# Kernel optimization log

Measured on AMD Instinct MI355X. Metric: run time of the kernel, lower is better.

Reference implementation:

```python
import jax, jax.numpy as jnp
import numpy as np

N, E, B, H = 20000, 100000, 512, 64
IN_CH, EDGE_DIM, OUT_CH = 16, 8, 1


def setup_inputs() -> dict:
    key = jax.random.key(0)
    ks = jax.random.split(key, 20)
    rn = lambda k, shp, s=0.1: (jax.random.normal(k, shp, jnp.float32) * s)
    return {
        'x': rn(ks[0], (N, IN_CH), 1.0),
        'edge_index': jax.random.randint(ks[1], (2, E), 0, N),
        'edge_attr': rn(ks[2], (E, EDGE_DIM), 1.0),
        'batch': jnp.sort(jax.random.randint(ks[3], (N,), 0, B)),
        'lin0_w': rn(ks[4], (IN_CH, H)), 'lin0_b': jnp.zeros((H,), jnp.float32),
        'nn1_w': rn(ks[5], (EDGE_DIM, 128)), 'nn1_b': jnp.zeros((128,), jnp.float32),
        'nn2_w': rn(ks[6], (128, H * H), 0.02), 'nn2_b': jnp.zeros((H * H,), jnp.float32),
        'root_w': rn(ks[7], (H, H)), 'root_b': jnp.zeros((H,), jnp.float32),
        'gru_wih': rn(ks[8], (H, 3 * H)), 'gru_whh': rn(ks[9], (H, 3 * H)),
        'gru_bih': jnp.zeros((3 * H,), jnp.float32), 'gru_bhh': jnp.zeros((3 * H,), jnp.float32),
        'lstm_wih': rn(ks[10], (2 * H, 4 * H)), 'lstm_whh': rn(ks[11], (H, 4 * H)),
        'lstm_bih': jnp.zeros((4 * H,), jnp.float32), 'lstm_bhh': jnp.zeros((4 * H,), jnp.float32),
        'lin1_w': rn(ks[12], (2 * H, H)), 'lin1_b': jnp.zeros((H,), jnp.float32),
        'lin2_w': rn(ks[13], (H, OUT_CH)), 'lin2_b': jnp.zeros((OUT_CH,), jnp.float32),
    }


def reference(x, edge_index, edge_attr, batch, lin0_w, lin0_b, nn1_w, nn1_b,
              nn2_w, nn2_b, root_w, root_b, gru_wih, gru_whh, gru_bih, gru_bhh,
              lstm_wih, lstm_whh, lstm_bih, lstm_bhh, lin1_w, lin1_b, lin2_w, lin2_b):
    src, dst = edge_index[0], edge_index[1]
    # edge network weights (shared across the 3 message-passing steps)
    ew = jax.nn.relu(edge_attr @ nn1_w + nn1_b) @ nn2_w + nn2_b  # [E, H*H]
    ew = ew.reshape(E, H, H)
    deg = jnp.maximum(jax.ops.segment_sum(jnp.ones((E,), x.dtype), dst, N), 1.0)

    out = jax.nn.relu(x @ lin0_w + lin0_b)  # [N, H]
    h = out
    for _ in range(3):
        # NNConv: gather src feats, per-edge matvec, scatter-mean to dst, + root linear
        msg = jnp.einsum('ei,eio->eo', out[src], ew)                  # [E, H]
        agg = jax.ops.segment_sum(msg, dst, N) / deg[:, None]          # [N, H]
        m = jax.nn.relu(agg + out @ root_w + root_b)
        # GRU cell (torch gate order r, z, n)
        gi = m @ gru_wih + gru_bih
        gh = h @ gru_whh + gru_bhh
        r = jax.nn.sigmoid(gi[:, :H] + gh[:, :H])
        z = jax.nn.sigmoid(gi[:, H:2 * H] + gh[:, H:2 * H])
        n = jnp.tanh(gi[:, 2 * H:] + r * gh[:, 2 * H:])
        h = (1.0 - z) * n + z * h
        out = h

    # Set2Set pooling, 3 processing steps (torch LSTM gate order i, f, g, o)
    q_star = jnp.zeros((B, 2 * H), x.dtype)
    hh = jnp.zeros((B, H), x.dtype)
    cc = jnp.zeros((B, H), x.dtype)
    for _ in range(3):
        g = q_star @ lstm_wih + hh @ lstm_whh + lstm_bih + lstm_bhh    # [B, 4H]
        i_g = jax.nn.sigmoid(g[:, :H])
        f_g = jax.nn.sigmoid(g[:, H:2 * H])
        g_g = jnp.tanh(g[:, 2 * H:3 * H])
        o_g = jax.nn.sigmoid(g[:, 3 * H:])
        cc = f_g * cc + i_g * g_g
        hh = o_g * jnp.tanh(cc)
        q = hh                                                          # [B, H]
        e = jnp.sum(out * q[batch], axis=-1)                            # [N]
        e_max = jax.ops.segment_max(e, batch, B)
        a = jnp.exp(e - e_max[batch])
        a = a / jax.ops.segment_sum(a, batch, B)[batch]
        rvec = jax.ops.segment_sum(a[:, None] * out, batch, B)          # [B, H]
        q_star = jnp.concatenate([q, rvec], axis=-1)

    y = jax.nn.relu(q_star @ lin1_w + lin1_b) @ lin2_w + lin2_b         # [B, 1]
    return y
```

## Files before the change

### kernel.cpp

```cpp
#include <hip/hip_runtime.h>
#include <hip/hip_bf16.h>
#include <hip/hip_fp16.h>
#include <cstddef>
#include <cstdint>

#define N_NODES 20000
#define N_EDGES 100000
#define N_BATCH 512

#define EPB 96
#define TS 6
#define ECAP 100032

typedef __attribute__((ext_vector_type(8))) short ushort8_t;
typedef __attribute__((ext_vector_type(8))) _Float16 f16x8;
typedef __attribute__((ext_vector_type(4))) float f32x4;

union F16x8U { f16x8 v; unsigned int u[4]; };

__device__ __forceinline__ float sigmoidf_(float x) { return 1.f / (1.f + expf(-x)); }
__device__ __forceinline__ unsigned short f2h(float x) {
    return __half_as_ushort(__float2half(x));
}
__device__ __forceinline__ float h2f(unsigned short s) {
    return __half2float(__ushort_as_half(s));
}

#define LIN0_BLOCKS 5000
#define BSW_BLOCKS 258
#define CNT_BLOCKS 391

__global__ __launch_bounds__(256) void prep1_kernel(
        const float* __restrict__ x, const float* __restrict__ l0w, const float* __restrict__ l0b,
        const float* __restrict__ w2, const float* __restrict__ b2,
        const int* __restrict__ ei,
        float* __restrict__ out, unsigned short* __restrict__ bsw,
        int* __restrict__ cnt, int E) {
    int bid = blockIdx.x, tid = threadIdx.x;
    if (bid < LIN0_BLOCKS) {
        int idx = bid * 256 + tid;
        int n = idx >> 6, j = idx & 63;
        float acc = l0b[j];
#pragma unroll
        for (int i = 0; i < 16; i++) acc += x[n * 16 + i] * l0w[i * 64 + j];
        out[idx] = fmaxf(acc, 0.f);
    } else if (bid < LIN0_BLOCKS + BSW_BLOCKS) {
        int idx = (bid - LIN0_BLOCKS) * 256 + tid;
        if (idx < 66048) {
            int l = idx & 63, oc = (idx >> 6) & 3, ks = idx >> 8;
            int o = oc * 16 + (l & 15);
            int kap0 = ks * 32 + 8 * (l >> 4);
#pragma unroll
            for (int j = 0; j < 8; ++j) {
                int kap = kap0 + j;
                int k = kap >> 6, i = kap & 63;
                float v = (k < 128) ? w2[(size_t)k * 4096 + i * 64 + o] : b2[i * 64 + o];
                bsw[(size_t)idx * 8 + j] = f2h(v);
            }
        }
    } else {
        int e = (bid - LIN0_BLOCKS - BSW_BLOCKS) * 256 + tid;
        if (e < E) atomicAdd(&cnt[ei[E + e]], 1);
    }
}

__global__ __launch_bounds__(1024) void scan_kernel(const int* __restrict__ cnt,
                                                    int* __restrict__ cstart,
                                                    int* __restrict__ cursor,
                                                    float* __restrict__ degf, int n) {
    __shared__ int part[1024];
    int t = threadIdx.x;
    int base = t * 20;
    int loc[20];
    int s = 0;
#pragma unroll
    for (int i = 0; i < 20; ++i) {
        int idx = base + i;
        int c = (idx < n) ? cnt[idx] : 0;
        loc[i] = s;
        s += c;
    }
    part[t] = s;
    __syncthreads();
    for (int off = 1; off < 1024; off <<= 1) {
        int v = (t >= off) ? part[t - off] : 0;
        __syncthreads();
        part[t] += v;
        __syncthreads();
    }
    int tb = part[t] - s;
#pragma unroll
    for (int i = 0; i < 20; ++i) {
        int idx = base + i;
        if (idx < n) {
            int b0 = tb + loc[i];
            cstart[idx] = b0;
            cursor[idx] = b0;
            degf[idx] = (float)cnt[idx];
        }
    }
}

__global__ void place_kernel(const int* __restrict__ ei, int* __restrict__ cursor,
                             int* __restrict__ eperm, int* __restrict__ src_s, int E) {
    int e = blockIdx.x * 256 + threadIdx.x;
    if (e < E) {
        int dst = ei[E + e];
        int slot = atomicAdd(&cursor[dst], 1);
        eperm[slot] = e;
        src_s[slot] = ei[e];
    }
}

__global__ __launch_bounds__(256) void hidden_kernel(const float* __restrict__ ea,
                                                     const float* __restrict__ w1,
                                                     const float* __restrict__ b1,
                                                     const int* __restrict__ eperm,
                                                     unsigned short* __restrict__ hb) {
    int idx = blockIdx.x * 256 + threadIdx.x;
    int s = idx >> 7, j = idx & 127;
    int e = eperm[s];
    float acc = b1[j];
#pragma unroll
    for (int i = 0; i < 8; i++) acc += ea[e * 8 + i] * w1[i * 128 + j];
    hb[idx] = f2h(fmaxf(acc, 0.f));
}

__global__ __launch_bounds__(256, 2) void msg_mfma(const float* __restrict__ out,
                                                   const unsigned short* __restrict__ hb,
                                                   const unsigned short* __restrict__ bsw,
                                                   const int* __restrict__ src_s,
                                                   unsigned short* __restrict__ msgp, int E) {
    __shared__ __align__(16) unsigned short hs16[128 * EPB];
    const int tid = threadIdx.x;
    const int w = tid >> 6, l = tid & 63;
    const int e0 = blockIdx.x * EPB;
    const int r16 = l & 15, q = l >> 4;

    if (tid < EPB) {
        int e = e0 + tid;
        bool v = e < E;
        const ushort8_t* hrow = (const ushort8_t*)(hb + (size_t)e * 128);
#pragma unroll
        for (int c = 0; c < 16; ++c) {
            ushort8_t hv = {};
            if (v) hv = hrow[c];
#pragma unroll
            for (int j = 0; j < 8; ++j)
                hs16[(c * 8 + j) * EPB + tid] = (unsigned short)hv[j];
        }
    }

    f16x8 sfrag[TS][2];
#pragma unroll
    for (int t = 0; t < TS; ++t) {
        int e = e0 + t * 16 + r16;
        int src = (e < E) ? src_s[e] : 0;
        const f32x4* p = (const f32x4*)(out + (size_t)src * 64);
#pragma unroll
        for (int st = 0; st < 2; ++st) {
            f16x8 f = {};
            if (e < E) {
                f32x4 a = p[st * 8 + q * 2], b = p[st * 8 + q * 2 + 1];
#pragma unroll
                for (int j = 0; j < 4; ++j) { f[j] = (_Float16)a[j]; f[4 + j] = (_Float16)b[j]; }
            }
            sfrag[t][st] = f;
        }
    }

    const f16x8* bp = (const f16x8*)bsw;
    f16x8 bfA[8], bfB[8];
#pragma unroll
    for (int i = 0; i < 8; ++i) bfA[i] = bp[((w * 8 + i) << 6) + l];

    __syncthreads();

    f32x4 acc[TS][4] = {};

#define MSG_COMPUTE(K, BF)                                                     \
    {                                                                          \
        _Pragma("unroll")                                                      \
        for (int t = 0; t < TS; ++t) {                                         \
            unsigned int hu = hs16[(K) * EPB + t * 16 + r16];                  \
            _Pragma("unroll")                                                  \
            for (int st = 0; st < 2; ++st) {                                   \
                F16x8U s_, a_;                                                 \
                s_.v = sfrag[t][st];                                           \
                asm("v_pk_mul_f16 %0, %1, %2 op_sel:[0,0] op_sel_hi:[0,1]"     \
                    : "=v"(a_.u[0]) : "v"(hu), "v"(s_.u[0]));                  \
                asm("v_pk_mul_f16 %0, %1, %2 op_sel:[0,0] op_sel_hi:[0,1]"     \
                    : "=v"(a_.u[1]) : "v"(hu), "v"(s_.u[1]));                  \
                asm("v_pk_mul_f16 %0, %1, %2 op_sel:[0,0] op_sel_hi:[0,1]"     \
                    : "=v"(a_.u[2]) : "v"(hu), "v"(s_.u[2]));                  \
                asm("v_pk_mul_f16 %0, %1, %2 op_sel:[0,0] op_sel_hi:[0,1]"     \
                    : "=v"(a_.u[3]) : "v"(hu), "v"(s_.u[3]));                  \
                _Pragma("unroll")                                              \
                for (int oc = 0; oc < 4; ++oc)                                 \
                    acc[t][oc] = __builtin_amdgcn_mfma_f32_16x16x32_f16(       \
                        a_.v, BF[st * 4 + oc], acc[t][oc], 0, 0, 0);           \
            }                                                                  \
        }                                                                      \
    }

#pragma unroll 1
    for (int kk = 0; kk < 16; ++kk) {
        int k1 = w + kk * 8;
        int k2 = k1 + 4;
#pragma unroll
        for (int i = 0; i < 8; ++i) bfB[i] = bp[((k2 * 8 + i) << 6) + l];
        MSG_COMPUTE(k1, bfA);
        if (kk < 15) {
            int k3 = k1 + 8;
#pragma unroll
            for (int i = 0; i < 8; ++i) bfA[i] = bp[((k3 * 8 + i) << 6) + l];
        }
        MSG_COMPUTE(k2, bfB);
    }
#undef MSG_COMPUTE

    if (w == 0) {
#pragma unroll
        for (int i = 0; i < 8; ++i) bfA[i] = bp[((128 * 8 + i) << 6) + l];
#pragma unroll
        for (int t = 0; t < TS; ++t)
#pragma unroll
            for (int st = 0; st < 2; ++st)
#pragma unroll
                for (int oc = 0; oc < 4; ++oc)
                    acc[t][oc] = __builtin_amdgcn_mfma_f32_16x16x32_f16(
                        sfrag[t][st], bfA[st * 4 + oc], acc[t][oc], 0, 0, 0);
    }

    unsigned short* slab = msgp + (size_t)w * ECAP * 64;
#pragma unroll
    for (int t = 0; t < TS; ++t) {
#pragma unroll
        for (int r = 0; r < 4; ++r) {
            int e = e0 + t * 16 + q * 4 + r;
            if (e < E) {
                unsigned short* row = slab + (size_t)e * 64 + r16;
                row[0]  = f2h(acc[t][0][r]);
                row[16] = f2h(acc[t][1][r]);
                row[32] = f2h(acc[t][2][r]);
                row[48] = f2h(acc[t][3][r]);
            }
        }
    }
}

__global__ __launch_bounds__(256) void gru_kernel(float* __restrict__ out,
                                                  const unsigned short* __restrict__ msgp,
                                                  const int* __restrict__ cstart,
                                                  const int* __restrict__ cnt,
                                                  const float* __restrict__ deg,
                                                  const float* __restrict__ root_w,
                                                  const float* __restrict__ root_b,
                                                  const float* __restrict__ wih,
                                                  const float* __restrict__ whh,
                                                  const float* __restrict__ bih,
                                                  const float* __restrict__ bhh) {
    int w = threadIdx.x >> 6, j = threadIdx.x & 63;
    int n = blockIdx.x * 4 + w;
    __shared__ float s_o[4][64];
    __shared__ float s_m[4][64];
    s_o[w][j] = out[(size_t)n * 64 + j];
    __syncthreads();

    float msum = 0.f;
    {
        int base = cstart[n], c = cnt[n];
        for (int s2 = 0; s2 < c; ++s2) {
            size_t slot = (size_t)(base + s2) * 64 + j;
            float a0 = h2f(msgp[slot]);
            float a1 = h2f(msgp[(size_t)ECAP * 64 + slot]);
            float a2 = h2f(msgp[2 * (size_t)ECAP * 64 + slot]);
            float a3 = h2f(msgp[3 * (size_t)ECAP * 64 + slot]);
            msum += (a0 + a1) + (a2 + a3);
        }
    }
    float d = deg[n]; if (d < 1.f) d = 1.f;
    float mv = msum / d + root_b[j];
#pragma unroll 8
    for (int i = 0; i < 64; i++) mv += s_o[w][i] * root_w[i * 64 + j];
    mv = fmaxf(mv, 0.f);
    s_m[w][j] = mv;
    __syncthreads();
    float gi_r = bih[j], gi_z = bih[64 + j], gi_n = bih[128 + j];
    float gh_r = bhh[j], gh_z = bhh[64 + j], gh_n = bhh[128 + j];
#pragma unroll 4
    for (int i = 0; i < 64; i++) {
        float m = s_m[w][i], hv = s_o[w][i];
        gi_r += m * wih[i * 192 + j];
        gi_z += m * wih[i * 192 + 64 + j];
        gi_n += m * wih[i * 192 + 128 + j];
        gh_r += hv * whh[i * 192 + j];
        gh_z += hv * whh[i * 192 + 64 + j];
        gh_n += hv * whh[i * 192 + 128 + j];
    }
    float r = sigmoidf_(gi_r + gh_r);
    float z = sigmoidf_(gi_z + gh_z);
    float nn = tanhf(gi_n + r * gh_n);
    float hnew = (1.f - z) * nn + z * s_o[w][j];
    out[(size_t)n * 64 + j] = hnew;
}

__global__ __launch_bounds__(256) void s2s_final(const float* __restrict__ out,
                                                 const int* __restrict__ batch,
                                                 const float* __restrict__ wih,
                                                 const float* __restrict__ whh,
                                                 const float* __restrict__ bih,
                                                 const float* __restrict__ bhh,
                                                 const float* __restrict__ w1,
                                                 const float* __restrict__ b1,
                                                 const float* __restrict__ w2,
                                                 const float* __restrict__ b2,
                                                 float* __restrict__ y, int N) {
    int b = blockIdx.x;
    int tid = threadIdx.x;
    int gate = tid >> 6, j = tid & 63;
    __shared__ float s_qs[128];
    __shared__ float s_g[4][64];
    __shared__ float s_h[64];
    __shared__ float s_c[64];
    __shared__ int s_lo, s_hi;
    __shared__ float s_red[4];
    __shared__ float s_rv[4][64];

    if (tid < 128) s_qs[tid] = 0.f;
    if (gate == 2) s_h[j] = 0.f;
    if (gate == 3) s_c[j] = 0.f;
    if (tid == 0) {
        int lo = 0, hi = N;
        while (lo < hi) { int mid = (lo + hi) >> 1; if (batch[mid] < b) lo = mid + 1; else hi = mid; }
        s_lo = lo;
        int lo2 = lo, hi2 = N;
        while (lo2 < hi2) { int mid = (lo2 + hi2) >> 1; if (batch[mid] < b + 1) lo2 = mid + 1; else hi2 = mid; }
        s_hi = lo2;
    }
    __syncthreads();

    for (int it = 0; it < 3; ++it) {
        float g = bih[gate * 64 + j] + bhh[gate * 64 + j];
#pragma unroll 4
        for (int i = 0; i < 128; ++i) g += s_qs[i] * wih[i * 256 + gate * 64 + j];
#pragma unroll 4
        for (int i = 0; i < 64; ++i) g += s_h[i] * whh[i * 256 + gate * 64 + j];
        s_g[gate][j] = g;
        __syncthreads();
        if (gate == 0) {
            float c = sigmoidf_(s_g[1][j]) * s_c[j] + sigmoidf_(s_g[0][j]) * tanhf(s_g[2][j]);
            float h = sigmoidf_(s_g[3][j]) * tanhf(c);
            s_c[j] = c;
            s_h[j] = h;
            s_qs[j] = h;
        }
        __syncthreads();

        int lo = s_lo, hi = s_hi;
        float wmax = -3.402823e38f;
        for (int n = lo + gate; n < hi; n += 4) {
            float p = out[(size_t)n * 64 + j] * s_h[j];
#pragma unroll
            for (int d = 32; d >= 1; d >>= 1) p += __shfl_xor(p, d);
            wmax = fmaxf(wmax, p);
        }
        if (j == 0) s_red[gate] = wmax;
        __syncthreads();
        float m = fmaxf(fmaxf(s_red[0], s_red[1]), fmaxf(s_red[2], s_red[3]));
        __syncthreads();
        float ssum = 0.f, rv = 0.f;
        for (int n = lo + gate; n < hi; n += 4) {
            float xv = out[(size_t)n * 64 + j];
            float p = xv * s_h[j];
#pragma unroll
            for (int d = 32; d >= 1; d >>= 1) p += __shfl_xor(p, d);
            float a = expf(p - m);
            ssum += a;
            rv += a * xv;
        }
        if (j == 0) s_red[gate] = ssum;
        s_rv[gate][j] = rv;
        __syncthreads();
        if (gate == 0) {
            float S = s_red[0] + s_red[1] + s_red[2] + s_red[3];
            float r = s_rv[0][j] + s_rv[1][j] + s_rv[2][j] + s_rv[3][j];
            s_qs[64 + j] = (S > 0.f) ? r / S : 0.f;
        }
        __syncthreads();
    }

    if (gate == 0) {
        float tv = b1[j];
#pragma unroll 4
        for (int i = 0; i < 128; ++i) tv += s_qs[i] * w1[i * 64 + j];
        tv = fmaxf(tv, 0.f);
        float p = tv * w2[j];
#pragma unroll
        for (int d = 32; d >= 1; d >>= 1) p += __shfl_xor(p, d);
        if (j == 0) y[b] = p + b2[0];
    }
}

extern "C" void kernel_launch(void* const* d_in, const int* in_sizes, int n_in,
                              void* d_out, int out_size, void* d_ws, size_t ws_size,
                              hipStream_t stream) {
    const int N = N_NODES, E = N_EDGES, B = N_BATCH;
    const float* x       = (const float*)d_in[0];
    const int*   ei      = (const int*)d_in[1];
    const float* ea      = (const float*)d_in[2];
    const int*   batch   = (const int*)d_in[3];
    const float* lin0_w  = (const float*)d_in[4];
    const float* lin0_b  = (const float*)d_in[5];
    const float* nn1_w   = (const float*)d_in[6];
    const float* nn1_b   = (const float*)d_in[7];
    const float* nn2_w   = (const float*)d_in[8];
    const float* nn2_b   = (const float*)d_in[9];
    const float* root_w  = (const float*)d_in[10];
    const float* root_b  = (const float*)d_in[11];
    const float* gru_wih = (const float*)d_in[12];
    const float* gru_whh = (const float*)d_in[13];
    const float* gru_bih = (const float*)d_in[14];
    const float* gru_bhh = (const float*)d_in[15];
    const float* lstm_wih = (const float*)d_in[16];
    const float* lstm_whh = (const float*)d_in[17];
    const float* lstm_bih = (const float*)d_in[18];
    const float* lstm_bhh = (const float*)d_in[19];
    const float* lin1_w  = (const float*)d_in[20];
    const float* lin1_b  = (const float*)d_in[21];
    const float* lin2_w  = (const float*)d_in[22];
    const float* lin2_b  = (const float*)d_in[23];
    float* y = (float*)d_out;

    char* ws = (char*)d_ws;
    size_t off = 0;
    auto alloc = [&](size_t bytes) { void* p = ws + off; off = (off + bytes + 255) & ~(size_t)255; return p; };
    unsigned short* hb   = (unsigned short*)alloc((size_t)E * 128 * 2);
    unsigned short* bsw  = (unsigned short*)alloc((size_t)66048 * 8 * 2);
    unsigned short* msgp = (unsigned short*)alloc((size_t)4 * ECAP * 64 * 2);
    float* out    = (float*)alloc((size_t)N * 64 * 4);
    float* deg    = (float*)alloc((size_t)N * 4);
    int*   cnt    = (int*)alloc((size_t)N * 4);
    int*   cstart = (int*)alloc((size_t)N * 4);
    int*   cursor = (int*)alloc((size_t)N * 4);
    int*   eperm  = (int*)alloc((size_t)E * 4);
    int*   src_s  = (int*)alloc((size_t)E * 4);

    hipMemsetAsync(cnt, 0, (size_t)N * 4, stream);

    prep1_kernel<<<LIN0_BLOCKS + BSW_BLOCKS + CNT_BLOCKS, 256, 0, stream>>>(
        x, lin0_w, lin0_b, nn2_w, nn2_b, ei, out, bsw, cnt, E);
    scan_kernel<<<1, 1024, 0, stream>>>(cnt, cstart, cursor, deg, N);
    place_kernel<<<(E + 255) / 256, 256, 0, stream>>>(ei, cursor, eperm, src_s, E);
    hidden_kernel<<<E * 128 / 256, 256, 0, stream>>>(ea, nn1_w, nn1_b, eperm, hb);

    for (int step = 0; step < 3; ++step) {
        msg_mfma<<<(E + EPB - 1) / EPB, 256, 0, stream>>>(out, hb, bsw, src_s, msgp, E);
        gru_kernel<<<N / 4, 256, 0, stream>>>(out, msgp, cstart, cnt, deg, root_w, root_b,
                                              gru_wih, gru_whh, gru_bih, gru_bhh);
    }

    s2s_final<<<B, 256, 0, stream>>>(out, batch, lstm_wih, lstm_whh, lstm_bih, lstm_bhh,
                                     lin1_w, lin1_b, lin2_w, lin2_b, y, N);
}
```

Measured before the change: 707.4 us.

## Fuse edge hidden-layer computation into message kernel, drop hidden buffer

Removes the separate hidden_kernel and its E×128 fp16 hidden buffer. place_kernel now writes a dst-sorted copy of edge_attr, and each msg_mfma block recomputes relu(ea·W1+b1) into shared memory from weights staged in LDS. This removes the write and the three reads of the 25MB hidden buffer plus one launch, in exchange for recomputing the small 8×128 matvec in every step and adding LDS use and an extra barrier.

```diff
diff --git a/kernel.cpp b/kernel.cpp
--- a/kernel.cpp
+++ b/kernel.cpp
@@ -101,54 +101,40 @@
     }
 }
 
-__global__ void place_kernel(const int* __restrict__ ei, int* __restrict__ cursor,
-                             int* __restrict__ eperm, int* __restrict__ src_s, int E) {
+__global__ void place_kernel(const int* __restrict__ ei, const float* __restrict__ ea,
+                             int* __restrict__ cursor,
+                             int* __restrict__ src_s, float* __restrict__ ea_s, int E) {
     int e = blockIdx.x * 256 + threadIdx.x;
     if (e < E) {
         int dst = ei[E + e];
         int slot = atomicAdd(&cursor[dst], 1);
-        eperm[slot] = e;
         src_s[slot] = ei[e];
-    }
-}
-
-__global__ __launch_bounds__(256) void hidden_kernel(const float* __restrict__ ea,
-                                                     const float* __restrict__ w1,
-                                                     const float* __restrict__ b1,
-                                                     const int* __restrict__ eperm,
-                                                     unsigned short* __restrict__ hb) {
-    int idx = blockIdx.x * 256 + threadIdx.x;
-    int s = idx >> 7, j = idx & 127;
-    int e = eperm[s];
-    float acc = b1[j];
-#pragma unroll
-    for (int i = 0; i < 8; i++) acc += ea[e * 8 + i] * w1[i * 128 + j];
-    hb[idx] = f2h(fmaxf(acc, 0.f));
+        const float4* s = (const float4*)(ea + (size_t)e * 8);
+        float4 a = s[0], b = s[1];
+        float4* d = (float4*)(ea_s + (size_t)slot * 8);
+        d[0] = a; d[1] = b;
+    }
 }
 
 __global__ __launch_bounds__(256, 2) void msg_mfma(const float* __restrict__ out,
-                                                   const unsigned short* __restrict__ hb,
+                                                   const float* __restrict__ ea_s,
+                                                   const float* __restrict__ w1g,
+                                                   const float* __restrict__ b1g,
                                                    const unsigned short* __restrict__ bsw,
                                                    const int* __restrict__ src_s,
                                                    unsigned short* __restrict__ msgp, int E) {
     __shared__ __align__(16) unsigned short hs16[128 * EPB];
+    __shared__ __align__(16) float w1l[8 * 128];
+    __shared__ __align__(16) float b1l[128];
     const int tid = threadIdx.x;
     const int w = tid >> 6, l = tid & 63;
     const int e0 = blockIdx.x * EPB;
     const int r16 = l & 15, q = l >> 4;
 
-    if (tid < EPB) {
-        int e = e0 + tid;
-        bool v = e < E;
-        const ushort8_t* hrow = (const ushort8_t*)(hb + (size_t)e * 128);
-#pragma unroll
-        for (int c = 0; c < 16; ++c) {
-            ushort8_t hv = {};
-            if (v) hv = hrow[c];
-#pragma unroll
-            for (int j = 0; j < 8; ++j)
-                hs16[(c * 8 + j) * EPB + tid] = (unsigned short)hv[j];
-        }
+    {
+        f32x4 v = *(const f32x4*)&w1g[tid * 4];
+        *(f32x4*)&w1l[tid * 4] = v;
+        if (tid < 32) *(f32x4*)&b1l[tid * 4] = *(const f32x4*)&b1g[tid * 4];
     }
 
     f16x8 sfrag[TS][2];
@@ -166,6 +152,32 @@
                 for (int j = 0; j < 4; ++j) { f[j] = (_Float16)a[j]; f[4 + j] = (_Float16)b[j]; }
             }
             sfrag[t][st] = f;
+        }
+    }
+
+    __syncthreads();
+
+    if (tid < 192) {
+        int ep = tid >> 1;
+        int koff = (tid & 1) * 64;
+        int e = e0 + ep;
+        bool v = e < E;
+        float ear[8];
+        const float* earow = ea_s + (size_t)(v ? e : 0) * 8;
+#pragma unroll
+        for (int i = 0; i < 8; ++i) ear[i] = earow[i];
+#pragma unroll
+        for (int kv = 0; kv < 16; ++kv) {
+            int k = koff + kv * 4;
+            f32x4 a = *(const f32x4*)&b1l[k];
+#pragma unroll
+            for (int i = 0; i < 8; ++i) {
+                f32x4 wv = *(const f32x4*)&w1l[i * 128 + k];
+                a += ear[i] * wv;
+            }
+#pragma unroll
+            for (int jj = 0; jj < 4; ++jj)
+                hs16[(k + jj) * EPB + ep] = v ? f2h(fmaxf(a[jj], 0.f)) : (unsigned short)0;
         }
     }
 
@@ -435,15 +447,14 @@
     char* ws = (char*)d_ws;
     size_t off = 0;
     auto alloc = [&](size_t bytes) { void* p = ws + off; off = (off + bytes + 255) & ~(size_t)255; return p; };
-    unsigned short* hb   = (unsigned short*)alloc((size_t)E * 128 * 2);
     unsigned short* bsw  = (unsigned short*)alloc((size_t)66048 * 8 * 2);
     unsigned short* msgp = (unsigned short*)alloc((size_t)4 * ECAP * 64 * 2);
+    float* ea_s   = (float*)alloc((size_t)ECAP * 8 * 4);
     float* out    = (float*)alloc((size_t)N * 64 * 4);
     float* deg    = (float*)alloc((size_t)N * 4);
     int*   cnt    = (int*)alloc((size_t)N * 4);
     int*   cstart = (int*)alloc((size_t)N * 4);
     int*   cursor = (int*)alloc((size_t)N * 4);
-    int*   eperm  = (int*)alloc((size_t)E * 4);
     int*   src_s  = (int*)alloc((size_t)E * 4);
 
     hipMemsetAsync(cnt, 0, (size_t)N * 4, stream);
@@ -451,11 +462,11 @@
     prep1_kernel<<<LIN0_BLOCKS + BSW_BLOCKS + CNT_BLOCKS, 256, 0, stream>>>(
         x, lin0_w, lin0_b, nn2_w, nn2_b, ei, out, bsw, cnt, E);
     scan_kernel<<<1, 1024, 0, stream>>>(cnt, cstart, cursor, deg, N);
-    place_kernel<<<(E + 255) / 256, 256, 0, stream>>>(ei, cursor, eperm, src_s, E);
-    hidden_kernel<<<E * 128 / 256, 256, 0, stream>>>(ea, nn1_w, nn1_b, eperm, hb);
+    place_kernel<<<(E + 255) / 256, 256, 0, stream>>>(ei, ea, cursor, src_s, ea_s, E);
 
     for (int step = 0; step < 3; ++step) {
-        msg_mfma<<<(E + EPB - 1) / EPB, 256, 0, stream>>>(out, hb, bsw, src_s, msgp, E);
+        msg_mfma<<<(E + EPB - 1) / EPB, 256, 0, stream>>>(out, ea_s, nn1_w, nn1_b,
+                                                          bsw, src_s, msgp, E);
         gru_kernel<<<N / 4, 256, 0, stream>>>(out, msgp, cstart, cnt, deg, root_w, root_b,
                                               gru_wih, gru_whh, gru_bih, gru_bhh);
     }
```

Result: faster. 671.7 us (median of 2 runs) (-5.0%).
